# Kernel tuning notes

Hardware: AMD Instinct MI355X
Metric: run time of the kernel (lower is better)

The kernel has to match this reference:

```python
import jax, jax.numpy as jnp
import numpy as np

B, T, E, S = 16, 2048, 1024, 2000
HID = 150
GI = 3 * E


def _mlp(x, W1, b1, W2, b2, W3, b3):
    # Score module: Linear->ReLU->(Dropout eval=id)->Linear->ReLU->(Dropout)->Linear(->1)
    h = jax.nn.relu(x @ W1 + b1)
    h = jax.nn.relu(h @ W2 + b2)
    return h @ W3 + b3


def setup_inputs() -> dict:
    key = jax.random.key(0)
    ks = jax.random.split(key, 16)
    batch_embeds = jax.random.normal(ks[0], (B, T, E), dtype=jnp.float32)
    starts = jnp.sort(jax.random.randint(ks[1], (B, S), 0, T - 33), axis=-1)
    lengths = jax.random.randint(ks[2], (B, S), 0, 24)
    num_spans = jax.random.randint(ks[3], (B,), 1, S + 1)
    sc = 0.02
    p = lambda k, shape: jax.random.normal(k, shape, dtype=jnp.float32) * sc
    return {
        "batch_embeds": batch_embeds,
        "starts": starts,
        "lengths": lengths,
        "num_spans": num_spans,
        "Wa1": p(ks[4], (E, HID)), "ba1": jnp.zeros((HID,), jnp.float32),
        "Wa2": p(ks[5], (HID, HID)), "ba2": jnp.zeros((HID,), jnp.float32),
        "Wa3": p(ks[6], (HID, 1)), "ba3": jnp.zeros((1,), jnp.float32),
        "Ws1": p(ks[7], (GI, HID)), "bs1": jnp.zeros((HID,), jnp.float32),
        "Ws2": p(ks[8], (HID, HID)), "bs2": jnp.zeros((HID,), jnp.float32),
        "Ws3": p(ks[9], (HID, 1)), "bs3": jnp.zeros((1,), jnp.float32),
    }


def reference(batch_embeds, starts, lengths, num_spans,
              Wa1, ba1, Wa2, ba2, Wa3, ba3,
              Ws1, bs1, Ws2, bs2, Ws3, bs3):
    # attention score per token: [B,T,1]
    attns = _mlp(batch_embeds, Wa1, ba1, Wa2, ba2, Wa3, ba3)
    weighted = batch_embeds * attns  # [B,T,E]
    # prefix sums turn the ragged per-span sum into two gathers per span
    csum = jnp.cumsum(weighted, axis=1)
    csum = jnp.concatenate([jnp.zeros_like(csum[:, :1]), csum], axis=1)  # [B,T+1,E]
    ends = starts + lengths  # inclusive end index, < T
    g_start = jnp.take_along_axis(batch_embeds, starts[..., None], axis=1)  # [B,S,E]
    g_end = jnp.take_along_axis(batch_embeds, ends[..., None], axis=1)      # [B,S,E]
    span_sum = (jnp.take_along_axis(csum, (ends + 1)[..., None], axis=1)
                - jnp.take_along_axis(csum, starts[..., None], axis=1))     # [B,S,E]
    span_emb = jnp.concatenate([g_start, g_end, span_sum], axis=-1)  # [B,S,3E]
    # zero-pad spans beyond each document's span count (matches torch zeros padding)
    mask = (jnp.arange(span_emb.shape[1])[None, :] < num_spans[:, None])[..., None]
    span_emb = jnp.where(mask, span_emb, jnp.zeros((), span_emb.dtype))
    mention_scores = _mlp(span_emb, Ws1, bs1, Ws2, bs2, Ws3, bs3)  # [B,S,1]
    return span_emb, mention_scores
```

## Files before the change

### kernel.cpp

```cpp
#include <hip/hip_runtime.h>
#include <hip/hip_bf16.h>

#define B_   16
#define T_   2048
#define E_   1024
#define S_   2000
#define HID_ 150
#define GI_  3072

typedef __attribute__((ext_vector_type(8))) short short8;
typedef __attribute__((ext_vector_type(4))) float f32x4;

constexpr int NPAD  = 160;
constexpr int LSTR  = 168;
constexpr int MROWS = 64;

__device__ __forceinline__ void gload16(const void* gsrc, void* ldst) {
    __builtin_amdgcn_global_load_lds(
        (const __attribute__((address_space(1))) unsigned int*)gsrc,
        (__attribute__((address_space(3))) unsigned int*)ldst,
        16, 0, 0);
}

__device__ __forceinline__ short8 pack8(float4 a, float4 b) {
    union { __hip_bfloat162 h[4]; short8 s; } u;
    u.h[0] = __float22bfloat162_rn(make_float2(a.x, a.y));
    u.h[1] = __float22bfloat162_rn(make_float2(a.z, a.w));
    u.h[2] = __float22bfloat162_rn(make_float2(b.x, b.y));
    u.h[3] = __float22bfloat162_rn(make_float2(b.z, b.w));
    return u.s;
}

__device__ __forceinline__ short8 pack8v(f32x4 a, f32x4 b) {
    union { __hip_bfloat162 h[4]; short8 s; } u;
    u.h[0] = __float22bfloat162_rn(make_float2(a.x, a.y));
    u.h[1] = __float22bfloat162_rn(make_float2(a.z, a.w));
    u.h[2] = __float22bfloat162_rn(make_float2(b.x, b.y));
    u.h[3] = __float22bfloat162_rn(make_float2(b.z, b.w));
    return u.s;
}

__global__ __launch_bounds__(256)
void transpose_all(const float* __restrict__ Wa1, const float* __restrict__ Wa2,
                   const float* __restrict__ Ws1, const float* __restrict__ Ws2,
                   __hip_bfloat16* __restrict__ Wt1a, __hip_bfloat16* __restrict__ Wt2a,
                   __hip_bfloat16* __restrict__ Wt1s, __hip_bfloat16* __restrict__ Wt2s)
{
    const int s0 = 160 * 1024, s1 = 160 * 160, s2 = 160 * 3072, s3 = 160 * 160;
    int i = blockIdx.x * 256 + threadIdx.x;
    if (i < s0) {
        int n = i >> 10, k = i & 1023;
        Wt1a[i] = __float2bfloat16(n < HID_ ? Wa1[k * HID_ + n] : 0.f);
    } else if (i < s0 + s1) {
        int j = i - s0, n = j / 160, k = j - n * 160;
        Wt2a[j] = __float2bfloat16((n < HID_ && k < HID_) ? Wa2[k * HID_ + n] : 0.f);
    } else if (i < s0 + s1 + s2) {
        int j = i - s0 - s1, n = j / 3072, k = j - n * 3072;
        Wt1s[j] = __float2bfloat16(n < HID_ ? Ws1[k * HID_ + n] : 0.f);
    } else if (i < s0 + s1 + s2 + s3) {
        int j = i - s0 - s1 - s2, n = j / 160, k = j - n * 160;
        Wt2s[j] = __float2bfloat16((n < HID_ && k < HID_) ? Ws2[k * HID_ + n] : 0.f);
    }
}

template<int K1>
__global__ __launch_bounds__(256, 2)
void mlp_mfma(const float* __restrict__ xin,
              const __hip_bfloat16* __restrict__ Wt1, const float* __restrict__ b1,
              const __hip_bfloat16* __restrict__ Wt2, const float* __restrict__ b2,
              const float* __restrict__ W3, const float* __restrict__ b3,
              float* __restrict__ outp)
{
    constexpr int NC  = K1 / 64;
    constexpr int ACH = 64 * 64 * 4;
    constexpr int BCH = 160 * 64 * 2;
    __shared__ __align__(16) char smem[2 * ACH + 2 * BCH];

    const int tid  = threadIdx.x;
    const int lane = tid & 63;
    const int w    = tid >> 6;
    const int rg   = w >> 1;
    const int cg   = w & 1;
    const int lr   = lane & 15;
    const int hi   = lane >> 4;

    const long long row0 = (long long)blockIdx.x * MROWS;

    auto stageA = [&](int bi, int c) {
        char* dst = smem + bi * ACH;
#pragma unroll
        for (int j = 0; j < 4; ++j) {
            const int row  = (w * 4 + j) * 4 + (lane >> 4);
            const int slot = (lane & 15) ^ (row & 7);
            gload16(xin + (row0 + row) * (long long)K1 + c * 64 + slot * 4,
                    dst + (w * 4 + j) * 1024);
        }
    };
    auto stageB = [&](int bi, int c) {
        char* dst = smem + 2 * ACH + bi * BCH;
#pragma unroll
        for (int j = 0; j < 5; ++j) {
            const int nrow = (w * 5 + j) * 8 + (lane >> 3);
            const int slot = (lane & 7) ^ (nrow & 7);
            gload16(Wt1 + (long long)nrow * K1 + c * 64 + slot * 8,
                    dst + (w * 5 + j) * 1024);
        }
    };

    f32x4 acc[2][5];
#pragma unroll
    for (int rt = 0; rt < 2; ++rt)
#pragma unroll
        for (int nt = 0; nt < 5; ++nt) acc[rt][nt] = (f32x4){0.f, 0.f, 0.f, 0.f};

    stageA(0, 0);
    stageB(0, 0);

    for (int c = 0; c < NC; ++c) {
        __syncthreads();
        if (c + 1 < NC) { stageA((c + 1) & 1, c + 1); stageB((c + 1) & 1, c + 1); }
        const int bi = c & 1;
        const char* sA = smem + bi * ACH;
        const char* sB = smem + 2 * ACH + bi * BCH;
#pragma unroll
        for (int ks = 0; ks < 2; ++ks) {
            short8 bfr[5];
#pragma unroll
            for (int nt = 0; nt < 5; ++nt) {
                const int nrow = cg * 80 + nt * 16 + lr;
                const int slot = (ks * 4 + hi) ^ (nrow & 7);
                bfr[nt] = *(const short8*)(sB + nrow * 128 + slot * 16);
            }
#pragma unroll
            for (int rt = 0; rt < 2; ++rt) {
                const int r = rg * 32 + rt * 16 + lr;
                const int s0i = (ks * 8 + hi * 2) ^ (r & 7);
                const int s1i = (ks * 8 + hi * 2 + 1) ^ (r & 7);
                float4 a0 = *(const float4*)(sA + r * 256 + s0i * 16);
                float4 a1 = *(const float4*)(sA + r * 256 + s1i * 16);
                short8 afr = pack8(a0, a1);
#pragma unroll
                for (int nt = 0; nt < 5; ++nt)
                    acc[rt][nt] = __builtin_amdgcn_mfma_f32_16x16x32_bf16(
                        afr, bfr[nt], acc[rt][nt], 0, 0, 0);
            }
        }
    }
    __syncthreads();

    __hip_bfloat16* hl = (__hip_bfloat16*)smem;

#pragma unroll
    for (int nt = 0; nt < 5; ++nt) {
        const int ch = cg * 80 + nt * 16 + lr;
        const float bb = (ch < HID_) ? b1[ch] : 0.f;
#pragma unroll
        for (int rt = 0; rt < 2; ++rt)
#pragma unroll
            for (int r4 = 0; r4 < 4; ++r4) {
                const int row = rg * 32 + rt * 16 + hi * 4 + r4;
                float h = acc[rt][nt][r4] + bb;
                hl[row * LSTR + ch] = __float2bfloat16(h > 0.f ? h : 0.f);
            }
    }
    __syncthreads();

    f32x4 acc2[2][5];
#pragma unroll
    for (int rt = 0; rt < 2; ++rt)
#pragma unroll
        for (int nt = 0; nt < 5; ++nt) acc2[rt][nt] = (f32x4){0.f, 0.f, 0.f, 0.f};

#pragma unroll
    for (int ks = 0; ks < 5; ++ks) {
        const int k0 = ks * 32 + hi * 8;
        short8 bfr[5];
#pragma unroll
        for (int nt = 0; nt < 5; ++nt)
            bfr[nt] = *(const short8*)(Wt2 + (cg * 80 + nt * 16 + lr) * NPAD + k0);
#pragma unroll
        for (int rt = 0; rt < 2; ++rt) {
            short8 afr = *(const short8*)&hl[(rg * 32 + rt * 16 + lr) * LSTR + k0];
#pragma unroll
            for (int nt = 0; nt < 5; ++nt)
                acc2[rt][nt] = __builtin_amdgcn_mfma_f32_16x16x32_bf16(
                    afr, bfr[nt], acc2[rt][nt], 0, 0, 0);
        }
    }
    __syncthreads();

#pragma unroll
    for (int nt = 0; nt < 5; ++nt) {
        const int ch = cg * 80 + nt * 16 + lr;
        const float bb = (ch < HID_) ? b2[ch] : 0.f;
#pragma unroll
        for (int rt = 0; rt < 2; ++rt)
#pragma unroll
            for (int r4 = 0; r4 < 4; ++r4) {
                const int row = rg * 32 + rt * 16 + hi * 4 + r4;
                float h = acc2[rt][nt][r4] + bb;
                hl[row * LSTR + ch] = __float2bfloat16(h > 0.f ? h : 0.f);
            }
    }
    __syncthreads();

    {
        const int row = tid >> 2, quad = tid & 3;
        const int kb = quad * 38;
        const int ke = (kb + 38 > HID_) ? HID_ : kb + 38;
        float s = 0.f;
        for (int k = kb; k < ke; ++k)
            s += __bfloat162float(hl[row * LSTR + k]) * W3[k];
        s += __shfl_xor(s, 1);
        s += __shfl_xor(s, 2);
        if (quad == 0) outp[row0 + row] = s + b3[0];
    }
}

__global__ __launch_bounds__(512, 4)
void span_score(const float* __restrict__ x, const float* __restrict__ attn,
                const int* __restrict__ starts, const int* __restrict__ lengths,
                const int* __restrict__ nspans,
                const __hip_bfloat16* __restrict__ Wt1, const float* __restrict__ b1,
                const __hip_bfloat16* __restrict__ Wt2, const float* __restrict__ b2,
                const float* __restrict__ W3, const float* __restrict__ b3,
                float* __restrict__ spanout, float* __restrict__ scoreout)
{
    __shared__ __align__(16) char smem[58112];
    int* stL = (int*)(smem + 57344);
    int* enL = (int*)(smem + 57600);
    int* bL  = (int*)(smem + 57856);

    const int tid  = threadIdx.x;
    const int lane = tid & 63;
    const int w    = tid >> 6;
    const int rg   = w >> 1;
    const int cg   = w & 1;
    const int lr   = lane & 15;
    const int hi   = lane >> 4;

    int bid = blockIdx.x;
    {
        const int qq = 500 / 8, rr = 500 % 8;
        const int xcd = bid % 8, i = bid / 8;
        bid = (xcd < rr ? xcd * (qq + 1) : rr * (qq + 1) + (xcd - rr) * qq) + i;
    }
    const int span0 = bid * 64;

    if (tid < 64) {
        const int sp = span0 + tid;
        const int b  = sp / S_;
        const int s  = sp - b * S_;
        const bool val = s < nspans[b];
        const int st = val ? starts[sp] : 0;
        stL[tid] = st;
        enL[tid] = val ? (st + lengths[sp]) : -1;
        bL[tid]  = b;
    }
    __syncthreads();

    const int r    = tid >> 3;
    const int q    = tid & 7;
    const int st_r = stL[r];
    const int en_r = enL[r];
    const long long sp_r = span0 + r;
    const float* xb = x + (long long)bL[r] * T_ * E_;
    const float* ab = attn + bL[r] * T_;

    auto constructA = [&](int bi, int c) {
        f32x4 v0 = (f32x4){0.f, 0.f, 0.f, 0.f};
        f32x4 v1 = (f32x4){0.f, 0.f, 0.f, 0.f};
        if (c < 32) {
            if (en_r >= st_r) {
                const int srow = (c < 16) ? st_r : en_r;
                const float* p = xb + (long long)srow * E_ + (c & 15) * 64 + q * 8;
                v0 = *(const f32x4*)p;
                v1 = *(const f32x4*)(p + 4);
            }
        } else if (en_r >= st_r) {
            const int cl = (c - 32) * 64 + q * 8;
            const float* p0 = xb + (long long)st_r * E_ + cl;
            f32x4 a0 = v0, a1 = v0, b0 = v0, b1 = v0;
#pragma unroll 4
            for (int u = 0; u < 24; ++u) {
                const float wv = (st_r + u <= en_r) ? ab[st_r + u] : 0.f;
                const f32x4 u0 = *(const f32x4*)(p0 + u * E_);
                const f32x4 u1 = *(const f32x4*)(p0 + u * E_ + 4);
                if (u & 1) { b0 += u0 * wv; b1 += u1 * wv; }
                else       { a0 += u0 * wv; a1 += u1 * wv; }
            }
            v0 = a0 + b0;
            v1 = a1 + b1;
        }
        float* orow = spanout + sp_r * (3 * E_) + c * 64 + q * 8;
        *(f32x4*)orow       = v0;
        *(f32x4*)(orow + 4) = v1;
        *(short8*)(smem + bi * 8192 + r * 128 + ((q ^ (r & 7)) * 16)) = pack8v(v0, v1);
    };

    auto stageB = [&](int bi, int c) {
        char* dst = smem + 16384 + bi * 20480;
#pragma unroll
        for (int j = 0; j < 3; ++j) {
            const int idx = w * 3 + j;
            if (idx < 20) {
                const int nrow = idx * 8 + (lane >> 3);
                const int slot = (lane & 7) ^ (nrow & 7);
                gload16(Wt1 + (long long)nrow * GI_ + c * 64 + slot * 8,
                        dst + idx * 1024);
            }
        }
    };

    f32x4 acc[5];
#pragma unroll
    for (int nt = 0; nt < 5; ++nt) acc[nt] = (f32x4){0.f, 0.f, 0.f, 0.f};

    constructA(0, 0);
    stageB(0, 0);

    for (int c = 0; c < 48; ++c) {
        __syncthreads();
        if (c + 1 < 48) stageB((c + 1) & 1, c + 1);
        const int bi = c & 1;
        const char* sAc = smem + bi * 8192;
        const char* sBc = smem + 16384 + bi * 20480;
#pragma unroll
        for (int ks = 0; ks < 2; ++ks) {
            short8 bfr[5];
#pragma unroll
            for (int nt = 0; nt < 5; ++nt) {
                const int nrow = cg * 80 + nt * 16 + lr;
                const int slot = (ks * 4 + hi) ^ (nrow & 7);
                bfr[nt] = *(const short8*)(sBc + nrow * 128 + slot * 16);
            }
            const int r2 = rg * 16 + lr;
            const int sl = (ks * 4 + hi) ^ (r2 & 7);
            short8 afr = *(const short8*)(sAc + r2 * 128 + sl * 16);
#pragma unroll
            for (int nt = 0; nt < 5; ++nt)
                acc[nt] = __builtin_amdgcn_mfma_f32_16x16x32_bf16(
                    afr, bfr[nt], acc[nt], 0, 0, 0);
        }
        if (c + 1 < 48) constructA((c + 1) & 1, c + 1);
    }
    __syncthreads();

    __hip_bfloat16* hl = (__hip_bfloat16*)smem;

#pragma unroll
    for (int nt = 0; nt < 5; ++nt) {
        const int ch = cg * 80 + nt * 16 + lr;
        const float bb = (ch < HID_) ? b1[ch] : 0.f;
#pragma unroll
        for (int r4 = 0; r4 < 4; ++r4) {
            const int row = rg * 16 + hi * 4 + r4;
            float h = acc[nt][r4] + bb;
            hl[row * LSTR + ch] = __float2bfloat16(h > 0.f ? h : 0.f);
        }
    }
    __syncthreads();

    f32x4 acc2[5];
#pragma unroll
    for (int nt = 0; nt < 5; ++nt) acc2[nt] = (f32x4){0.f, 0.f, 0.f, 0.f};

#pragma unroll
    for (int ks = 0; ks < 5; ++ks) {
        const int k0 = ks * 32 + hi * 8;
        short8 bfr[5];
#pragma unroll
        for (int nt = 0; nt < 5; ++nt)
            bfr[nt] = *(const short8*)(Wt2 + (cg * 80 + nt * 16 + lr) * NPAD + k0);
        short8 afr = *(const short8*)&hl[(rg * 16 + lr) * LSTR + k0];
#pragma unroll
        for (int nt = 0; nt < 5; ++nt)
            acc2[nt] = __builtin_amdgcn_mfma_f32_16x16x32_bf16(
                afr, bfr[nt], acc2[nt], 0, 0, 0);
    }
    __syncthreads();

#pragma unroll
    for (int nt = 0; nt < 5; ++nt) {
        const int ch = cg * 80 + nt * 16 + lr;
        const float bb = (ch < HID_) ? b2[ch] : 0.f;
#pragma unroll
        for (int r4 = 0; r4 < 4; ++r4) {
            const int row = rg * 16 + hi * 4 + r4;
            float h = acc2[nt][r4] + bb;
            hl[row * LSTR + ch] = __float2bfloat16(h > 0.f ? h : 0.f);
        }
    }
    __syncthreads();

    {
        const int row = tid >> 3, oct = tid & 7;
        const int kb = oct * 19;
        const int ke = (kb + 19 > HID_) ? HID_ : kb + 19;
        float s = 0.f;
        for (int k = kb; k < ke; ++k)
            s += __bfloat162float(hl[row * LSTR + k]) * W3[k];
        s += __shfl_xor(s, 1);
        s += __shfl_xor(s, 2);
        s += __shfl_xor(s, 4);
        if (oct == 0) scoreout[span0 + row] = s + b3[0];
    }
}

extern "C" void kernel_launch(void* const* d_in, const int* in_sizes, int n_in,
                              void* d_out, int out_size, void* d_ws, size_t ws_size,
                              hipStream_t stream) {
    const float* x       = (const float*)d_in[0];
    const int*   starts  = (const int*)d_in[1];
    const int*   lengths = (const int*)d_in[2];
    const int*   nspans  = (const int*)d_in[3];
    const float* Wa1 = (const float*)d_in[4];
    const float* ba1 = (const float*)d_in[5];
    const float* Wa2 = (const float*)d_in[6];
    const float* ba2 = (const float*)d_in[7];
    const float* Wa3 = (const float*)d_in[8];
    const float* ba3 = (const float*)d_in[9];
    const float* Ws1 = (const float*)d_in[10];
    const float* bs1 = (const float*)d_in[11];
    const float* Ws2 = (const float*)d_in[12];
    const float* bs2 = (const float*)d_in[13];
    const float* Ws3 = (const float*)d_in[14];
    const float* bs3 = (const float*)d_in[15];

    float* out        = (float*)d_out;
    float* out_scores = out + (long long)B_ * S_ * 3 * E_;

    char* ws = (char*)d_ws;
    float*          attn = (float*)ws;
    __hip_bfloat16* Wt1a = (__hip_bfloat16*)(ws + 131072);
    __hip_bfloat16* Wt2a = (__hip_bfloat16*)(ws + 458752);
    __hip_bfloat16* Wt1s = (__hip_bfloat16*)(ws + 509952);
    __hip_bfloat16* Wt2s = (__hip_bfloat16*)(ws + 1492992);

    transpose_all<<<2760, 256, 0, stream>>>(Wa1, Wa2, Ws1, Ws2,
                                            Wt1a, Wt2a, Wt1s, Wt2s);

    mlp_mfma<E_><<<(B_ * T_) / MROWS, 256, 0, stream>>>
        (x, Wt1a, ba1, Wt2a, ba2, Wa3, ba3, attn);

    span_score<<<500, 512, 0, stream>>>
        (x, attn, starts, lengths, nspans,
         Wt1s, bs1, Wt2s, bs2, Ws3, bs3, out, out_scores);
}
```

Before: 271.6 us.

## Replace per-span weighted token loop with precomputed prefix-sum lookups

Adds two kernels that build a full weighted cumulative sum over tokens: per-tile partial sums first, then a tiled scan. The span kernel then reads the span_sum as one or two prefix rows instead of looping over up to 24 tokens with attention weights. The aim is to cut the redundant per-span gather and FMA work. In exchange it adds a full read of x twice and a write of a 128MB csum buffer, and the prefix difference can lose some float precision.

```diff
diff --git a/kernel.cpp b/kernel.cpp
--- a/kernel.cpp
+++ b/kernel.cpp
@@ -217,8 +217,43 @@
     }
 }
 
+__global__ __launch_bounds__(256)
+void wsum_tiles(const float* __restrict__ x, const float* __restrict__ attn,
+                float* __restrict__ P)
+{
+    const int b = blockIdx.x >> 5, tile = blockIdx.x & 31, q = threadIdx.x;
+    const float* xb = x + ((long long)b * T_ + tile * 64) * E_ + q * 4;
+    const float* ab = attn + b * T_ + tile * 64;
+    f32x4 a0 = (f32x4){0.f, 0.f, 0.f, 0.f}, a1 = a0;
+#pragma unroll 8
+    for (int t = 0; t < 64; t += 2) {
+        a0 += ab[t]     * *(const f32x4*)(xb + (long long)t * E_);
+        a1 += ab[t + 1] * *(const f32x4*)(xb + (long long)(t + 1) * E_);
+    }
+    *(f32x4*)(P + ((long long)(b * 32 + tile)) * E_ + q * 4) = a0 + a1;
+}
+
+__global__ __launch_bounds__(256)
+void wcumsum(const float* __restrict__ x, const float* __restrict__ attn,
+             const float* __restrict__ P, float* __restrict__ csum)
+{
+    const int b = blockIdx.x >> 5, tile = blockIdx.x & 31, q = threadIdx.x;
+    f32x4 pfx = (f32x4){0.f, 0.f, 0.f, 0.f};
+    for (int tau = 0; tau < tile; ++tau)
+        pfx += *(const f32x4*)(P + ((long long)(b * 32 + tau)) * E_ + q * 4);
+    const float* xb = x + ((long long)b * T_ + tile * 64) * E_ + q * 4;
+    float*       cb = csum + ((long long)b * T_ + tile * 64) * E_ + q * 4;
+    const float* ab = attn + b * T_ + tile * 64;
+    f32x4 acc = pfx;
+#pragma unroll 4
+    for (int t = 0; t < 64; ++t) {
+        acc += ab[t] * *(const f32x4*)(xb + (long long)t * E_);
+        *(f32x4*)(cb + (long long)t * E_) = acc;
+    }
+}
+
 __global__ __launch_bounds__(512, 4)
-void span_score(const float* __restrict__ x, const float* __restrict__ attn,
+void span_score(const float* __restrict__ x, const float* __restrict__ csum,
                 const int* __restrict__ starts, const int* __restrict__ lengths,
                 const int* __restrict__ nspans,
                 const __hip_bfloat16* __restrict__ Wt1, const float* __restrict__ b1,
@@ -264,8 +299,8 @@
     const int st_r = stL[r];
     const int en_r = enL[r];
     const long long sp_r = span0 + r;
-    const float* xb = x + (long long)bL[r] * T_ * E_;
-    const float* ab = attn + bL[r] * T_;
+    const float* xb = x    + (long long)bL[r] * T_ * E_;
+    const float* cb = csum + (long long)bL[r] * T_ * E_;
 
     auto constructA = [&](int bi, int c) {
         f32x4 v0 = (f32x4){0.f, 0.f, 0.f, 0.f};
@@ -279,18 +314,14 @@
             }
         } else if (en_r >= st_r) {
             const int cl = (c - 32) * 64 + q * 8;
-            const float* p0 = xb + (long long)st_r * E_ + cl;
-            f32x4 a0 = v0, a1 = v0, b0 = v0, b1 = v0;
-#pragma unroll 4
-            for (int u = 0; u < 24; ++u) {
-                const float wv = (st_r + u <= en_r) ? ab[st_r + u] : 0.f;
-                const f32x4 u0 = *(const f32x4*)(p0 + u * E_);
-                const f32x4 u1 = *(const f32x4*)(p0 + u * E_ + 4);
-                if (u & 1) { b0 += u0 * wv; b1 += u1 * wv; }
-                else       { a0 += u0 * wv; a1 += u1 * wv; }
-            }
-            v0 = a0 + b0;
-            v1 = a1 + b1;
+            const float* pe = cb + (long long)en_r * E_ + cl;
+            v0 = *(const f32x4*)pe;
+            v1 = *(const f32x4*)(pe + 4);
+            if (st_r > 0) {
+                const float* ps = cb + (long long)(st_r - 1) * E_ + cl;
+                v0 -= *(const f32x4*)ps;
+                v1 -= *(const f32x4*)(ps + 4);
+            }
         }
         float* orow = spanout + sp_r * (3 * E_) + c * 64 + q * 8;
         *(f32x4*)orow       = v0;
@@ -436,6 +467,8 @@
     __hip_bfloat16* Wt2a = (__hip_bfloat16*)(ws + 458752);
     __hip_bfloat16* Wt1s = (__hip_bfloat16*)(ws + 509952);
     __hip_bfloat16* Wt2s = (__hip_bfloat16*)(ws + 1492992);
+    float*          Ptile = (float*)(ws + 2097152);
+    float*          csum  = (float*)(ws + 4194304);
 
     transpose_all<<<2760, 256, 0, stream>>>(Wa1, Wa2, Ws1, Ws2,
                                             Wt1a, Wt2a, Wt1s, Wt2s);
@@ -443,7 +476,10 @@
     mlp_mfma<E_><<<(B_ * T_) / MROWS, 256, 0, stream>>>
         (x, Wt1a, ba1, Wt2a, ba2, Wa3, ba3, attn);
 
+    wsum_tiles<<<B_ * 32, 256, 0, stream>>>(x, attn, Ptile);
+    wcumsum   <<<B_ * 32, 256, 0, stream>>>(x, attn, Ptile, csum);
+
     span_score<<<500, 512, 0, stream>>>
-        (x, attn, starts, lengths, nspans,
+        (x, csum, starts, lengths, nspans,
          Wt1s, bs1, Wt2s, bs2, Ws3, bs3, out, out_scores);
 }
```

After: 296.3 us. +9.1%, slower.
